# Performance work log

Measured on AMD Instinct MI355X. Metric: run time of the kernel, lower is better.

## Reference

```python
import jax, jax.numpy as jnp
import numpy as np

NSX, NSY = 8, 8          # subdomain grid
BATCH = 8                # PDE instances
PTS = 100_000            # points per instance
IN_C, HID, OUT_C = 32, 64, 32
NUM_CLUSTERS = BATCH * NSX * NSY  # 512


def _clusters(coords, batch_ids):
    # coords assumed in [0,1]^2; bucket into NSX x NSY grid per batch sample
    ix = jnp.clip((coords[:, 0] * NSX).astype(jnp.int32), 0, NSX - 1)
    iy = jnp.clip((coords[:, 1] * NSY).astype(jnp.int32), 0, NSY - 1)
    return batch_ids * (NSX * NSY) + iy * NSX + ix


def _mlp(h, W1, b1, W2, b2):
    # Linear -> GELU(exact, matches torch nn.GELU default) -> Linear
    return jax.nn.gelu(h @ W1 + b1, approximate=False) @ W2 + b2


def setup_inputs() -> dict:
    key = jax.random.key(0)
    ks = jax.random.split(key, 12)
    N = BATCH * PTS
    x = jax.random.normal(ks[0], (N, IN_C), dtype=jnp.float32)
    src_coords = jax.random.uniform(ks[1], (N, 2), dtype=jnp.float32)
    tgt_coords = jax.random.uniform(ks[2], (N, 2), dtype=jnp.float32)
    src_batch = jnp.repeat(jnp.arange(BATCH, dtype=jnp.int32), PTS)
    tgt_batch = jnp.repeat(jnp.arange(BATCH, dtype=jnp.int32), PTS)
    def lin(k, fan_in, fan_out):
        s = 1.0 / np.sqrt(fan_in)
        kw, kb = jax.random.split(k)
        W = jax.random.uniform(kw, (fan_in, fan_out), minval=-s, maxval=s, dtype=jnp.float32)
        b = jax.random.uniform(kb, (fan_out,), minval=-s, maxval=s, dtype=jnp.float32)
        return W, b
    Wv1, bv1 = lin(ks[3], IN_C, HID)
    Wv2, bv2 = lin(ks[4], HID, HID)
    Wt1, bt1 = lin(ks[5], 2 + HID, HID)
    Wt2, bt2 = lin(ks[6], HID, OUT_C)
    return {"x": x, "src_coords": src_coords, "src_batch": src_batch,
            "tgt_coords": tgt_coords, "tgt_batch": tgt_batch,
            "Wv1": Wv1, "bv1": bv1, "Wv2": Wv2, "bv2": bv2,
            "Wt1": Wt1, "bt1": bt1, "Wt2": Wt2, "bt2": bt2}


def reference(x, src_coords, src_batch, tgt_coords, tgt_batch,
              Wv1, bv1, Wv2, bv2, Wt1, bt1, Wt2, bt2):
    src_cl = _clusters(src_coords, src_batch)        # [Ns]
    tgt_cl = _clusters(tgt_coords, tgt_batch)        # [Nt]
    h = _mlp(x, Wv1, bv1, Wv2, bv2)                  # [Ns, HID]
    # subdomain mean-pool (the integral over each subdomain)
    s = jax.ops.segment_sum(h, src_cl, num_segments=NUM_CLUSTERS)        # [C, HID]
    cnt = jax.ops.segment_sum(jnp.ones((h.shape[0], 1), h.dtype), src_cl,
                              num_segments=NUM_CLUSTERS)                 # [C, 1]
    pooled = s / jnp.maximum(cnt, 1.0)
    # broadcast pooled feature to each target point, concat target coords
    feat = jnp.concatenate([tgt_coords, pooled[tgt_cl]], axis=-1)        # [Nt, 2+HID]
    return _mlp(feat, Wt1, bt1, Wt2, bt2)            # [Nt, OUT_C]
```

## Files before the change

### kernel.cpp

```cpp
#include <hip/hip_runtime.h>

#define NC   512
#define INC  32
#define HID  64
#define OUTC 32
#define STRZ 68
#define GSTR 36
#define TSTR 40

typedef __attribute__((ext_vector_type(8))) __bf16 bf16x8;
typedef __attribute__((ext_vector_type(4))) __bf16 bf16x4;
typedef __attribute__((ext_vector_type(4))) float  f32x4;
typedef __attribute__((ext_vector_type(8))) float  f32x8;
typedef __attribute__((ext_vector_type(8))) unsigned int   u32x8;
typedef __attribute__((ext_vector_type(8))) unsigned short u16x8;
typedef __attribute__((ext_vector_type(4))) unsigned short u16x4;

static __device__ __forceinline__ f32x4 mfma16(bf16x8 a, bf16x8 b, f32x4 c){
    return __builtin_amdgcn_mfma_f32_16x16x32_bf16(a, b, c, 0, 0, 0);
}

__device__ __forceinline__ float gelu_f(float v){
    const float s  = v * 0.70710678118654752f;
    const float as = fabsf(s);
    const float t  = __builtin_amdgcn_rcpf(__builtin_fmaf(0.47047f, as, 1.0f));
    const float e  = __expf(-as * as);
    float p = __builtin_fmaf(0.7478556f, t, -0.0958798f);
    p = __builtin_fmaf(p, t, 0.3480242f);
    p = p * t;
    float er = __builtin_fmaf(-p, e, 1.0f);
    er = copysignf(er, s);
    return 0.5f * v * (1.0f + er);
}

__device__ __forceinline__ void split8v(f32x8 x, bf16x8& hi, bf16x8& lo){
    u32x8 ux = __builtin_bit_cast(u32x8, x);
    f32x8 hf = __builtin_bit_cast(f32x8, ux & 0xFFFF0000u);
    f32x8 lf = x - hf;
    u32x8 ul = __builtin_bit_cast(u32x8, lf);
    hi = __builtin_bit_cast(bf16x8, __builtin_convertvector(ux >> 16, u16x8));
    lo = __builtin_bit_cast(bf16x8, __builtin_convertvector(ul >> 16, u16x8));
}

__device__ __forceinline__ u16x4 pack4(f32x4 g){
    return __builtin_bit_cast(u16x4, __builtin_convertvector(g, bf16x4));
}

__global__ __launch_bounds__(256, 3) void k_src(
    const float* __restrict__ x, const float* __restrict__ sc,
    const float* __restrict__ Wv1, const float* __restrict__ bv1,
    float* __restrict__ partial, float* __restrict__ pcntf,
    int npb, int T, int bpb)
{
    __shared__ ushort gbuf[2][4][64][GSTR];
    __shared__ ushort lcw[2][4][32];
    const int t = threadIdx.x;
    const int wave = t >> 6, lane = t & 63;
    const int lrow = lane & 15, lgrp = lane >> 4;
    const int batch = blockIdx.x / bpb;
    const int pb    = blockIdx.x % bpb;

    bf16x8 Bh0, Bh1, Bh2, Bh3, Bl0, Bl1, Bl2, Bl3;
    float bnt0, bnt1, bnt2, bnt3;
    {
        f32x8 w;
        #pragma unroll
        for (int j = 0; j < 8; j++) w[j] = Wv1[(8*lgrp + j)*HID +  0 + lrow];
        split8v(w, Bh0, Bl0);  bnt0 = bv1[ 0 + lrow];
        #pragma unroll
        for (int j = 0; j < 8; j++) w[j] = Wv1[(8*lgrp + j)*HID + 16 + lrow];
        split8v(w, Bh1, Bl1);  bnt1 = bv1[16 + lrow];
        #pragma unroll
        for (int j = 0; j < 8; j++) w[j] = Wv1[(8*lgrp + j)*HID + 32 + lrow];
        split8v(w, Bh2, Bl2);  bnt2 = bv1[32 + lrow];
        #pragma unroll
        for (int j = 0; j < 8; j++) w[j] = Wv1[(8*lgrp + j)*HID + 48 + lrow];
        split8v(w, Bh3, Bl3);  bnt3 = bv1[48 + lrow];
    }
    u16x8 onesu;
    #pragma unroll
    for (int j = 0; j < 8; j++) onesu[j] = 0x3F80u;
    const bf16x8 ONE = __builtin_bit_cast(bf16x8, onesu);

    f32x4 P0 = (f32x4){0.f,0.f,0.f,0.f}, P1 = P0, P2 = P0, P3 = P0, C = P0;

    const int base   = batch * npb + pb * T * 16;
    const int PAIRS  = T >> 1;
    const int rounds = (PAIRS + 3) >> 2;

    int  p_cur  = wave;
    bool a_cur  = p_cur < PAIRS;
    float2 sA_c, sB_c; f32x8 xA_c, xB_c;
    if (a_cur){
        const int pt0 = base + p_cur * 32;
        sA_c = ((const float2*)sc)[pt0 + lrow];
        sB_c = ((const float2*)sc)[pt0 + 16 + lrow];
        xA_c = *(const f32x8*)(x + (size_t)(pt0 + lrow)*INC + 8*lgrp);
        xB_c = *(const f32x8*)(x + (size_t)(pt0 + 16 + lrow)*INC + 8*lgrp);
    }

    for (int r = 0; r < rounds; r++){
        const int buf = r & 1;
        const int  p_nxt = p_cur + 4;
        const bool a_nxt = p_nxt < PAIRS;
        float2 sA_n, sB_n; f32x8 xA_n, xB_n;
        if (a_nxt){
            const int pt0 = base + p_nxt * 32;
            sA_n = ((const float2*)sc)[pt0 + lrow];
            sB_n = ((const float2*)sc)[pt0 + 16 + lrow];
            xA_n = *(const f32x8*)(x + (size_t)(pt0 + lrow)*INC + 8*lgrp);
            xB_n = *(const f32x8*)(x + (size_t)(pt0 + 16 + lrow)*INC + 8*lgrp);
        }

        if (a_cur){
            int ixA = (int)(sA_c.x * 8.0f); ixA = ixA < 0 ? 0 : (ixA > 7 ? 7 : ixA);
            int iyA = (int)(sA_c.y * 8.0f); iyA = iyA < 0 ? 0 : (iyA > 7 ? 7 : iyA);
            int ixB = (int)(sB_c.x * 8.0f); ixB = ixB < 0 ? 0 : (ixB > 7 ? 7 : ixB);
            int iyB = (int)(sB_c.y * 8.0f); iyB = iyB < 0 ? 0 : (iyB > 7 ? 7 : iyB);
            if (lgrp == 0){
                lcw[buf][wave][lrow]      = (ushort)((iyA << 3) + ixA);
                lcw[buf][wave][16 + lrow] = (ushort)((iyB << 3) + ixB);
            }
            {
                bf16x8 Ah = __builtin_convertvector(xA_c, bf16x8);
                f32x4 a0 = (f32x4){0.f,0.f,0.f,0.f}, a1 = a0, a2 = a0, a3 = a0;
                a0 = mfma16(Ah, Bl0, a0); a1 = mfma16(Ah, Bl1, a1);
                a2 = mfma16(Ah, Bl2, a2); a3 = mfma16(Ah, Bl3, a3);
                a0 = mfma16(Ah, Bh0, a0); a1 = mfma16(Ah, Bh1, a1);
                a2 = mfma16(Ah, Bh2, a2); a3 = mfma16(Ah, Bh3, a3);
                f32x4 gv;
                gv[0]=gelu_f(a0[0]+bnt0); gv[1]=gelu_f(a0[1]+bnt0);
                gv[2]=gelu_f(a0[2]+bnt0); gv[3]=gelu_f(a0[3]+bnt0);
                *(u16x4*)&gbuf[buf][wave][ 0 + lrow][4*lgrp] = pack4(gv);
                gv[0]=gelu_f(a1[0]+bnt1); gv[1]=gelu_f(a1[1]+bnt1);
                gv[2]=gelu_f(a1[2]+bnt1); gv[3]=gelu_f(a1[3]+bnt1);
                *(u16x4*)&gbuf[buf][wave][16 + lrow][4*lgrp] = pack4(gv);
                gv[0]=gelu_f(a2[0]+bnt2); gv[1]=gelu_f(a2[1]+bnt2);
                gv[2]=gelu_f(a2[2]+bnt2); gv[3]=gelu_f(a2[3]+bnt2);
                *(u16x4*)&gbuf[buf][wave][32 + lrow][4*lgrp] = pack4(gv);
                gv[0]=gelu_f(a3[0]+bnt3); gv[1]=gelu_f(a3[1]+bnt3);
                gv[2]=gelu_f(a3[2]+bnt3); gv[3]=gelu_f(a3[3]+bnt3);
                *(u16x4*)&gbuf[buf][wave][48 + lrow][4*lgrp] = pack4(gv);
            }
            {
                bf16x8 Ah = __builtin_convertvector(xB_c, bf16x8);
                f32x4 a0 = (f32x4){0.f,0.f,0.f,0.f}, a1 = a0, a2 = a0, a3 = a0;
                a0 = mfma16(Ah, Bl0, a0); a1 = mfma16(Ah, Bl1, a1);
                a2 = mfma16(Ah, Bl2, a2); a3 = mfma16(Ah, Bl3, a3);
                a0 = mfma16(Ah, Bh0, a0); a1 = mfma16(Ah, Bh1, a1);
                a2 = mfma16(Ah, Bh2, a2); a3 = mfma16(Ah, Bh3, a3);
                f32x4 gv;
                gv[0]=gelu_f(a0[0]+bnt0); gv[1]=gelu_f(a0[1]+bnt0);
                gv[2]=gelu_f(a0[2]+bnt0); gv[3]=gelu_f(a0[3]+bnt0);
                *(u16x4*)&gbuf[buf][wave][ 0 + lrow][16 + 4*lgrp] = pack4(gv);
                gv[0]=gelu_f(a1[0]+bnt1); gv[1]=gelu_f(a1[1]+bnt1);
                gv[2]=gelu_f(a1[2]+bnt1); gv[3]=gelu_f(a1[3]+bnt1);
                *(u16x4*)&gbuf[buf][wave][16 + lrow][16 + 4*lgrp] = pack4(gv);
                gv[0]=gelu_f(a2[0]+bnt2); gv[1]=gelu_f(a2[1]+bnt2);
                gv[2]=gelu_f(a2[2]+bnt2); gv[3]=gelu_f(a2[3]+bnt2);
                *(u16x4*)&gbuf[buf][wave][32 + lrow][16 + 4*lgrp] = pack4(gv);
                gv[0]=gelu_f(a3[0]+bnt3); gv[1]=gelu_f(a3[1]+bnt3);
                gv[2]=gelu_f(a3[2]+bnt3); gv[3]=gelu_f(a3[3]+bnt3);
                *(u16x4*)&gbuf[buf][wave][48 + lrow][16 + 4*lgrp] = pack4(gv);
            }
        } else {
            if (lgrp == 0){
                lcw[buf][wave][lrow]      = 0xFFFFu;
                lcw[buf][wave][16 + lrow] = 0xFFFFu;
            }
            u16x4 zz = (u16x4){0,0,0,0};
            #pragma unroll
            for (int nt = 0; nt < 4; nt++){
                *(u16x4*)&gbuf[buf][wave][16*nt + lrow][4*lgrp] = zz;
                *(u16x4*)&gbuf[buf][wave][16*nt + lrow][16 + 4*lgrp] = zz;
            }
        }
        __syncthreads();

        const ushort tgt = (ushort)(16*wave + lrow);
        #pragma unroll
        for (int s = 0; s < 4; s++){
            const u16x8 lcv = *(const u16x8*)&lcw[buf][s][8*lgrp];
            u16x8 ohu;
            #pragma unroll
            for (int j = 0; j < 8; j++)
                ohu[j] = (lcv[j] == tgt) ? (ushort)0x3F80u : (ushort)0;
            const bf16x8 oh = __builtin_bit_cast(bf16x8, ohu);
            u16x4 glo, ghi;
            glo = *(const u16x4*)&gbuf[buf][s][ 0 + lrow][8*lgrp];
            ghi = *(const u16x4*)&gbuf[buf][s][ 0 + lrow][8*lgrp + 4];
            bf16x8 g0 = __builtin_bit_cast(bf16x8, __builtin_shufflevector(glo, ghi, 0,1,2,3,4,5,6,7));
            glo = *(const u16x4*)&gbuf[buf][s][16 + lrow][8*lgrp];
            ghi = *(const u16x4*)&gbuf[buf][s][16 + lrow][8*lgrp + 4];
            bf16x8 g1 = __builtin_bit_cast(bf16x8, __builtin_shufflevector(glo, ghi, 0,1,2,3,4,5,6,7));
            glo = *(const u16x4*)&gbuf[buf][s][32 + lrow][8*lgrp];
            ghi = *(const u16x4*)&gbuf[buf][s][32 + lrow][8*lgrp + 4];
            bf16x8 g2 = __builtin_bit_cast(bf16x8, __builtin_shufflevector(glo, ghi, 0,1,2,3,4,5,6,7));
            glo = *(const u16x4*)&gbuf[buf][s][48 + lrow][8*lgrp];
            ghi = *(const u16x4*)&gbuf[buf][s][48 + lrow][8*lgrp + 4];
            bf16x8 g3 = __builtin_bit_cast(bf16x8, __builtin_shufflevector(glo, ghi, 0,1,2,3,4,5,6,7));
            P0 = mfma16(oh, g0, P0);
            P1 = mfma16(oh, g1, P1);
            P2 = mfma16(oh, g2, P2);
            P3 = mfma16(oh, g3, P3);
            C  = mfma16(oh, ONE, C);
        }

        p_cur = p_nxt; a_cur = a_nxt;
        sA_c = sA_n; sB_c = sB_n; xA_c = xA_n; xB_c = xB_n;
    }

    float* dst = partial + (size_t)blockIdx.x * 4096;
    #pragma unroll
    for (int reg = 0; reg < 4; reg++){
        const int row = 16*wave + 4*lgrp + reg;
        dst[row*64 +  0 + lrow] = P0[reg];
        dst[row*64 + 16 + lrow] = P1[reg];
        dst[row*64 + 32 + lrow] = P2[reg];
        dst[row*64 + 48 + lrow] = P3[reg];
    }
    if (lrow == 0){
        #pragma unroll
        for (int reg = 0; reg < 4; reg++)
            pcntf[(size_t)blockIdx.x*64 + 16*wave + 4*lgrp + reg] = C[reg];
    }
}

__global__ __launch_bounds__(256) void k_cluster(
    const float* __restrict__ partial, const float* __restrict__ pcntf,
    const float* __restrict__ Wv2, const float* __restrict__ bv2,
    const float* __restrict__ Wt1, const float* __restrict__ bt1,
    float* __restrict__ z, int spb)
{
    __shared__ float red[4][HID];
    __shared__ float redn[4];
    __shared__ float m[HID];
    __shared__ float ph[HID];
    const int c = blockIdx.x;
    const int t = threadIdx.x, j = t & 63, sl = t >> 6;
    const int batch = c >> 6, lc = c & 63;

    float s = 0.0f, cn = 0.0f;
    for (int b = sl; b < spb; b += 4){
        const size_t slot = (size_t)batch * spb + b;
        s  += partial[slot * 4096 + (size_t)lc * 64 + j];
        cn += pcntf[slot * 64 + lc];
    }
    red[sl][j] = s;
    if (j == 0) redn[sl] = cn;
    __syncthreads();

    if (sl == 0){
        float stot = red[0][j] + red[1][j] + red[2][j] + red[3][j];
        float ntot = redn[0] + redn[1] + redn[2] + redn[3];
        const float inv = (ntot > 0.0f) ? (1.0f / ntot) : 0.0f;
        m[j] = stot * inv;
        __builtin_amdgcn_s_barrier();
        float a = bv2[j];
        #pragma unroll 8
        for (int i = 0; i < HID; i++) a += m[i] * Wv2[i*HID + j];
        if (ntot <= 0.0f) a = 0.0f;
        ph[j] = a;
        __builtin_amdgcn_s_barrier();
        float b = bt1[j];
        #pragma unroll 8
        for (int i = 0; i < HID; i++) b += ph[i] * Wt1[(2 + i)*HID + j];
        z[c*HID + j] = b;
    }
}

__global__ __launch_bounds__(256, 3) void k_tgt(
    const float* __restrict__ tc,
    const float* __restrict__ z, const float* __restrict__ Wt1,
    const float* __restrict__ Wt2, const float* __restrict__ bt2,
    float* __restrict__ out, int npb, int TT, int bpt)
{
    __shared__ float zs[64*STRZ];
    __shared__ __align__(16) float trans[4][16][TSTR];
    const int t = threadIdx.x;
    const int wave = t >> 6, lane = t & 63;
    const int lrow = lane & 15, lgrp = lane >> 4;
    const int batch = blockIdx.x / bpt;
    const int toff  = (blockIdx.x % bpt) * TT;

    for (int k = t; k < 4096; k += 256)
        zs[(k >> 6)*STRZ + (k & 63)] = z[(size_t)(batch*64)*HID + k];

    bf16x8 Bh00, Bh01, Bh10, Bh11, Bl00, Bl01, Bl10, Bl11;
    f32x8 w0v0, w0v1, w1v0, w1v1;
    {
        f32x8 w;
        #pragma unroll
        for (int j = 0; j < 8; j++) w[j] = Wt2[( 0 + 8*lgrp + j)*OUTC +  0 + lrow];
        split8v(w, Bh00, Bl00);
        #pragma unroll
        for (int j = 0; j < 8; j++) w[j] = Wt2[( 0 + 8*lgrp + j)*OUTC + 16 + lrow];
        split8v(w, Bh01, Bl01);
        #pragma unroll
        for (int j = 0; j < 8; j++) w[j] = Wt2[(32 + 8*lgrp + j)*OUTC +  0 + lrow];
        split8v(w, Bh10, Bl10);
        #pragma unroll
        for (int j = 0; j < 8; j++) w[j] = Wt2[(32 + 8*lgrp + j)*OUTC + 16 + lrow];
        split8v(w, Bh11, Bl11);
        #pragma unroll
        for (int j = 0; j < 8; j++){
            w0v0[j] = Wt1[ 0 + 8*lgrp + j];
            w0v1[j] = Wt1[32 + 8*lgrp + j];
            w1v0[j] = Wt1[HID +  0 + 8*lgrp + j];
            w1v1[j] = Wt1[HID + 32 + 8*lgrp + j];
        }
    }
    const float bo0 = bt2[lrow], bo1 = bt2[16 + lrow];
    __syncthreads();

    const size_t pbase = (size_t)batch * npb;
    float2 c2_c = ((const float2*)tc)[pbase + (size_t)(toff + wave)*16 + lrow];

    const int rpt = lane >> 3;
    const int rko = (lane & 7) * 4;

    for (int tt = toff + wave; tt < toff + TT; tt += 4){
        const int ttn = tt + 4;
        float2 c2_n = c2_c;
        if (ttn < toff + TT)
            c2_n = ((const float2*)tc)[pbase + (size_t)ttn*16 + lrow];

        int ix = (int)(c2_c.x * 8.0f); ix = ix < 0 ? 0 : (ix > 7 ? 7 : ix);
        int iy = (int)(c2_c.y * 8.0f); iy = iy < 0 ? 0 : (iy > 7 ? 7 : iy);
        const int zb = ((iy << 3) + ix) * STRZ;

        f32x8 z0 = *(const f32x8*)(&zs[zb +  0 + 8*lgrp]);
        f32x8 z1 = *(const f32x8*)(&zs[zb + 32 + 8*lgrp]);
        f32x8 g0, g1;
        #pragma unroll
        for (int j = 0; j < 8; j++){
            g0[j] = gelu_f(z0[j] + c2_c.x * w0v0[j] + c2_c.y * w1v0[j]);
            g1[j] = gelu_f(z1[j] + c2_c.x * w0v1[j] + c2_c.y * w1v1[j]);
        }
        bf16x8 Ah0, Al0, Ah1, Al1;
        split8v(g0, Ah0, Al0);
        split8v(g1, Ah1, Al1);

        f32x4 a0 = (f32x4){0.f,0.f,0.f,0.f}, a1 = a0;
        a0 = mfma16(Al0, Bh00, a0); a1 = mfma16(Al0, Bh01, a1);
        a0 = mfma16(Ah0, Bl00, a0); a1 = mfma16(Ah0, Bl01, a1);
        a0 = mfma16(Ah0, Bh00, a0); a1 = mfma16(Ah0, Bh01, a1);
        a0 = mfma16(Al1, Bh10, a0); a1 = mfma16(Al1, Bh11, a1);
        a0 = mfma16(Ah1, Bl10, a0); a1 = mfma16(Ah1, Bl11, a1);
        a0 = mfma16(Ah1, Bh10, a0); a1 = mfma16(Ah1, Bh11, a1);

        #pragma unroll
        for (int q = 0; q < 4; q++){
            trans[wave][4*lgrp + q][lrow]      = a0[q] + bo0;
            trans[wave][4*lgrp + q][16 + lrow] = a1[q] + bo1;
        }
        const size_t prow = pbase + (size_t)tt*16;
        f32x4 v0 = *(const f32x4*)&trans[wave][rpt][rko];
        f32x4 v1 = *(const f32x4*)&trans[wave][8 + rpt][rko];
        *(f32x4*)(out + (prow + rpt)*OUTC + rko)     = v0;
        *(f32x4*)(out + (prow + 8 + rpt)*OUTC + rko) = v1;

        c2_c = c2_n;
    }
}

extern "C" void kernel_launch(void* const* d_in, const int* in_sizes, int n_in,
                              void* d_out, int out_size, void* d_ws, size_t ws_size,
                              hipStream_t stream)
{
    const float* x   = (const float*)d_in[0];
    const float* sc  = (const float*)d_in[1];
    const int*   sb  = (const int*)  d_in[2];  (void)sb;
    const float* tc  = (const float*)d_in[3];
    const int*   tb  = (const int*)  d_in[4];  (void)tb;
    const float* Wv1 = (const float*)d_in[5];
    const float* bv1 = (const float*)d_in[6];
    const float* Wv2 = (const float*)d_in[7];
    const float* bv2 = (const float*)d_in[8];
    const float* Wt1 = (const float*)d_in[9];
    const float* bt1 = (const float*)d_in[10];
    const float* Wt2 = (const float*)d_in[11];
    const float* bt2 = (const float*)d_in[12];
    float* out = (float*)d_out;

    const int n   = in_sizes[2];
    const int npb = n / 8;
    const int tiles_pb = npb / 16;

    int bpb = 1;
    const int cands[4] = {125, 25, 5, 1};
    for (int ci = 0; ci < 4; ci++){
        const int d = cands[ci];
        if (tiles_pb % d) continue;
        if ((tiles_pb / d) & 1) continue;
        const size_t slots = (size_t)8 * d;
        const size_t need  = slots * 4096 * 4 + slots * 64 * 4 + (size_t)NC*HID*4 + 4096;
        if (need <= ws_size){ bpb = d; break; }
    }
    const int T    = tiles_pb / bpb;
    const int nblk = 8 * bpb;
    const size_t slots = (size_t)nblk;

    char* ws = (char*)d_ws;
    float* partial = (float*)(ws);
    float* pcntf   = (float*)(ws + slots * 4096 * 4);
    float* z       = (float*)(ws + slots * 4096 * 4 + slots * 64 * 4);

    k_src    <<<nblk, 256, 0, stream>>>(x, sc, Wv1, bv1, partial, pcntf, npb, T, bpb);
    k_cluster<<<NC, 256, 0, stream>>>(partial, pcntf, Wv2, bv2, Wt1, bt1, z, bpb);

    int TT = 1;
    const int tcands[5] = {10, 25, 5, 2, 1};
    for (int ci = 0; ci < 5; ci++){
        if (tiles_pb % tcands[ci] == 0){ TT = tcands[ci]; break; }
    }
    const int bpt = tiles_pb / TT;
    k_tgt    <<<8*bpt, 256, 0, stream>>>(tc, z, Wt1, Wt2, bt2, out, npb, TT, bpt);
}
```

Baseline: 104.2 us.

## Support odd tile counts in source kernel to allow more blocks, drop LDS double buffer

The source kernel now handles an odd number of 16-point tiles per block by guarding the A and B halves of each pair separately. This lets the host pick 250 blocks per batch instead of 125, doubling the grid for better CU fill. The double-buffered LDS staging is replaced with a single buffer plus an extra barrier per round, which cuts shared memory use but adds a sync. The target kernel's tile-per-block preference also changes from 10 to 25.

Result: slower. 110.3 us (+5.9%).

```diff
diff --git a/kernel.cpp b/kernel.cpp
--- a/kernel.cpp
+++ b/kernel.cpp
@@ -52,8 +52,8 @@
     float* __restrict__ partial, float* __restrict__ pcntf,
     int npb, int T, int bpb)
 {
-    __shared__ ushort gbuf[2][4][64][GSTR];
-    __shared__ ushort lcw[2][4][32];
+    __shared__ ushort gbuf[4][64][GSTR];
+    __shared__ ushort lcw[4][32];
     const int t = threadIdx.x;
     const int wave = t >> 6, lane = t & 63;
     const int lrow = lane & 15, lgrp = lane >> 4;
@@ -85,119 +85,124 @@
     f32x4 P0 = (f32x4){0.f,0.f,0.f,0.f}, P1 = P0, P2 = P0, P3 = P0, C = P0;
 
     const int base   = batch * npb + pb * T * 16;
-    const int PAIRS  = T >> 1;
+    const int PAIRS  = (T + 1) >> 1;
     const int rounds = (PAIRS + 3) >> 2;
 
     int  p_cur  = wave;
-    bool a_cur  = p_cur < PAIRS;
+    bool aA_c = p_cur < PAIRS;
+    bool aB_c = (2*p_cur + 1) < T;
     float2 sA_c, sB_c; f32x8 xA_c, xB_c;
-    if (a_cur){
+    if (aA_c){
         const int pt0 = base + p_cur * 32;
         sA_c = ((const float2*)sc)[pt0 + lrow];
+        xA_c = *(const f32x8*)(x + (size_t)(pt0 + lrow)*INC + 8*lgrp);
+    }
+    if (aB_c){
+        const int pt0 = base + p_cur * 32;
         sB_c = ((const float2*)sc)[pt0 + 16 + lrow];
-        xA_c = *(const f32x8*)(x + (size_t)(pt0 + lrow)*INC + 8*lgrp);
         xB_c = *(const f32x8*)(x + (size_t)(pt0 + 16 + lrow)*INC + 8*lgrp);
     }
 
     for (int r = 0; r < rounds; r++){
-        const int buf = r & 1;
         const int  p_nxt = p_cur + 4;
-        const bool a_nxt = p_nxt < PAIRS;
+        const bool aA_n = p_nxt < PAIRS;
+        const bool aB_n = (2*p_nxt + 1) < T;
         float2 sA_n, sB_n; f32x8 xA_n, xB_n;
-        if (a_nxt){
+        if (aA_n){
             const int pt0 = base + p_nxt * 32;
             sA_n = ((const float2*)sc)[pt0 + lrow];
+            xA_n = *(const f32x8*)(x + (size_t)(pt0 + lrow)*INC + 8*lgrp);
+        }
+        if (aB_n){
+            const int pt0 = base + p_nxt * 32;
             sB_n = ((const float2*)sc)[pt0 + 16 + lrow];
-            xA_n = *(const f32x8*)(x + (size_t)(pt0 + lrow)*INC + 8*lgrp);
             xB_n = *(const f32x8*)(x + (size_t)(pt0 + 16 + lrow)*INC + 8*lgrp);
         }
 
-        if (a_cur){
+        if (aA_c){
             int ixA = (int)(sA_c.x * 8.0f); ixA = ixA < 0 ? 0 : (ixA > 7 ? 7 : ixA);
             int iyA = (int)(sA_c.y * 8.0f); iyA = iyA < 0 ? 0 : (iyA > 7 ? 7 : iyA);
+            if (lgrp == 0) lcw[wave][lrow] = (ushort)((iyA << 3) + ixA);
+            bf16x8 Ah = __builtin_convertvector(xA_c, bf16x8);
+            f32x4 a0 = (f32x4){0.f,0.f,0.f,0.f}, a1 = a0, a2 = a0, a3 = a0;
+            a0 = mfma16(Ah, Bl0, a0); a1 = mfma16(Ah, Bl1, a1);
+            a2 = mfma16(Ah, Bl2, a2); a3 = mfma16(Ah, Bl3, a3);
+            a0 = mfma16(Ah, Bh0, a0); a1 = mfma16(Ah, Bh1, a1);
+            a2 = mfma16(Ah, Bh2, a2); a3 = mfma16(Ah, Bh3, a3);
+            f32x4 gv;
+            gv[0]=gelu_f(a0[0]+bnt0); gv[1]=gelu_f(a0[1]+bnt0);
+            gv[2]=gelu_f(a0[2]+bnt0); gv[3]=gelu_f(a0[3]+bnt0);
+            *(u16x4*)&gbuf[wave][ 0 + lrow][4*lgrp] = pack4(gv);
+            gv[0]=gelu_f(a1[0]+bnt1); gv[1]=gelu_f(a1[1]+bnt1);
+            gv[2]=gelu_f(a1[2]+bnt1); gv[3]=gelu_f(a1[3]+bnt1);
+            *(u16x4*)&gbuf[wave][16 + lrow][4*lgrp] = pack4(gv);
+            gv[0]=gelu_f(a2[0]+bnt2); gv[1]=gelu_f(a2[1]+bnt2);
+            gv[2]=gelu_f(a2[2]+bnt2); gv[3]=gelu_f(a2[3]+bnt2);
+            *(u16x4*)&gbuf[wave][32 + lrow][4*lgrp] = pack4(gv);
+            gv[0]=gelu_f(a3[0]+bnt3); gv[1]=gelu_f(a3[1]+bnt3);
+            gv[2]=gelu_f(a3[2]+bnt3); gv[3]=gelu_f(a3[3]+bnt3);
+            *(u16x4*)&gbuf[wave][48 + lrow][4*lgrp] = pack4(gv);
+        } else {
+            if (lgrp == 0) lcw[wave][lrow] = 0xFFFFu;
+            u16x4 zz = (u16x4){0,0,0,0};
+            #pragma unroll
+            for (int nt = 0; nt < 4; nt++)
+                *(u16x4*)&gbuf[wave][16*nt + lrow][4*lgrp] = zz;
+        }
+        if (aB_c){
             int ixB = (int)(sB_c.x * 8.0f); ixB = ixB < 0 ? 0 : (ixB > 7 ? 7 : ixB);
             int iyB = (int)(sB_c.y * 8.0f); iyB = iyB < 0 ? 0 : (iyB > 7 ? 7 : iyB);
-            if (lgrp == 0){
-                lcw[buf][wave][lrow]      = (ushort)((iyA << 3) + ixA);
-                lcw[buf][wave][16 + lrow] = (ushort)((iyB << 3) + ixB);
-            }
-            {
-                bf16x8 Ah = __builtin_convertvector(xA_c, bf16x8);
-                f32x4 a0 = (f32x4){0.f,0.f,0.f,0.f}, a1 = a0, a2 = a0, a3 = a0;
-                a0 = mfma16(Ah, Bl0, a0); a1 = mfma16(Ah, Bl1, a1);
-                a2 = mfma16(Ah, Bl2, a2); a3 = mfma16(Ah, Bl3, a3);
-                a0 = mfma16(Ah, Bh0, a0); a1 = mfma16(Ah, Bh1, a1);
-                a2 = mfma16(Ah, Bh2, a2); a3 = mfma16(Ah, Bh3, a3);
-                f32x4 gv;
-                gv[0]=gelu_f(a0[0]+bnt0); gv[1]=gelu_f(a0[1]+bnt0);
-                gv[2]=gelu_f(a0[2]+bnt0); gv[3]=gelu_f(a0[3]+bnt0);
-                *(u16x4*)&gbuf[buf][wave][ 0 + lrow][4*lgrp] = pack4(gv);
-                gv[0]=gelu_f(a1[0]+bnt1); gv[1]=gelu_f(a1[1]+bnt1);
-                gv[2]=gelu_f(a1[2]+bnt1); gv[3]=gelu_f(a1[3]+bnt1);
-                *(u16x4*)&gbuf[buf][wave][16 + lrow][4*lgrp] = pack4(gv);
-                gv[0]=gelu_f(a2[0]+bnt2); gv[1]=gelu_f(a2[1]+bnt2);
-                gv[2]=gelu_f(a2[2]+bnt2); gv[3]=gelu_f(a2[3]+bnt2);
-                *(u16x4*)&gbuf[buf][wave][32 + lrow][4*lgrp] = pack4(gv);
-                gv[0]=gelu_f(a3[0]+bnt3); gv[1]=gelu_f(a3[1]+bnt3);
-                gv[2]=gelu_f(a3[2]+bnt3); gv[3]=gelu_f(a3[3]+bnt3);
-                *(u16x4*)&gbuf[buf][wave][48 + lrow][4*lgrp] = pack4(gv);
-            }
-            {
-                bf16x8 Ah = __builtin_convertvector(xB_c, bf16x8);
-                f32x4 a0 = (f32x4){0.f,0.f,0.f,0.f}, a1 = a0, a2 = a0, a3 = a0;
-                a0 = mfma16(Ah, Bl0, a0); a1 = mfma16(Ah, Bl1, a1);
-                a2 = mfma16(Ah, Bl2, a2); a3 = mfma16(Ah, Bl3, a3);
-                a0 = mfma16(Ah, Bh0, a0); a1 = mfma16(Ah, Bh1, a1);
-                a2 = mfma16(Ah, Bh2, a2); a3 = mfma16(Ah, Bh3, a3);
-                f32x4 gv;
-                gv[0]=gelu_f(a0[0]+bnt0); gv[1]=gelu_f(a0[1]+bnt0);
-                gv[2]=gelu_f(a0[2]+bnt0); gv[3]=gelu_f(a0[3]+bnt0);
-                *(u16x4*)&gbuf[buf][wave][ 0 + lrow][16 + 4*lgrp] = pack4(gv);
-                gv[0]=gelu_f(a1[0]+bnt1); gv[1]=gelu_f(a1[1]+bnt1);
-                gv[2]=gelu_f(a1[2]+bnt1); gv[3]=gelu_f(a1[3]+bnt1);
-                *(u16x4*)&gbuf[buf][wave][16 + lrow][16 + 4*lgrp] = pack4(gv);
-                gv[0]=gelu_f(a2[0]+bnt2); gv[1]=gelu_f(a2[1]+bnt2);
-                gv[2]=gelu_f(a2[2]+bnt2); gv[3]=gelu_f(a2[3]+bnt2);
-                *(u16x4*)&gbuf[buf][wave][32 + lrow][16 + 4*lgrp] = pack4(gv);
-                gv[0]=gelu_f(a3[0]+bnt3); gv[1]=gelu_f(a3[1]+bnt3);
-                gv[2]=gelu_f(a3[2]+bnt3); gv[3]=gelu_f(a3[3]+bnt3);
-                *(u16x4*)&gbuf[buf][wave][48 + lrow][16 + 4*lgrp] = pack4(gv);
-            }
+            if (lgrp == 0) lcw[wave][16 + lrow] = (ushort)((iyB << 3) + ixB);
+            bf16x8 Ah = __builtin_convertvector(xB_c, bf16x8);
+            f32x4 a0 = (f32x4){0.f,0.f,0.f,0.f}, a1 = a0, a2 = a0, a3 = a0;
+            a0 = mfma16(Ah, Bl0, a0); a1 = mfma16(Ah, Bl1, a1);
+            a2 = mfma16(Ah, Bl2, a2); a3 = mfma16(Ah, Bl3, a3);
+            a0 = mfma16(Ah, Bh0, a0); a1 = mfma16(Ah, Bh1, a1);
+            a2 = mfma16(Ah, Bh2, a2); a3 = mfma16(Ah, Bh3, a3);
+            f32x4 gv;
+            gv[0]=gelu_f(a0[0]+bnt0); gv[1]=gelu_f(a0[1]+bnt0);
+            gv[2]=gelu_f(a0[2]+bnt0); gv[3]=gelu_f(a0[3]+bnt0);
+            *(u16x4*)&gbuf[wave][ 0 + lrow][16 + 4*lgrp] = pack4(gv);
+            gv[0]=gelu_f(a1[0]+bnt1); gv[1]=gelu_f(a1[1]+bnt1);
+            gv[2]=gelu_f(a1[2]+bnt1); gv[3]=gelu_f(a1[3]+bnt1);
+            *(u16x4*)&gbuf[wave][16 + lrow][16 + 4*lgrp] = pack4(gv);
+            gv[0]=gelu_f(a2[0]+bnt2); gv[1]=gelu_f(a2[1]+bnt2);
+            gv[2]=gelu_f(a2[2]+bnt2); gv[3]=gelu_f(a2[3]+bnt2);
+            *(u16x4*)&gbuf[wave][32 + lrow][16 + 4*lgrp] = pack4(gv);
+            gv[0]=gelu_f(a3[0]+bnt3); gv[1]=gelu_f(a3[1]+bnt3);
+            gv[2]=gelu_f(a3[2]+bnt3); gv[3]=gelu_f(a3[3]+bnt3);
+            *(u16x4*)&gbuf[wave][48 + lrow][16 + 4*lgrp] = pack4(gv);
         } else {
-            if (lgrp == 0){
-                lcw[buf][wave][lrow]      = 0xFFFFu;
-                lcw[buf][wave][16 + lrow] = 0xFFFFu;
-            }
+            if (lgrp == 0) lcw[wave][16 + lrow] = 0xFFFFu;
             u16x4 zz = (u16x4){0,0,0,0};
             #pragma unroll
-            for (int nt = 0; nt < 4; nt++){
-                *(u16x4*)&gbuf[buf][wave][16*nt + lrow][4*lgrp] = zz;
-                *(u16x4*)&gbuf[buf][wave][16*nt + lrow][16 + 4*lgrp] = zz;
-            }
-        }
+            for (int nt = 0; nt < 4; nt++)
+                *(u16x4*)&gbuf[wave][16*nt + lrow][16 + 4*lgrp] = zz;
+        }
+
         __syncthreads();
 
         const ushort tgt = (ushort)(16*wave + lrow);
         #pragma unroll
         for (int s = 0; s < 4; s++){
-            const u16x8 lcv = *(const u16x8*)&lcw[buf][s][8*lgrp];
+            const u16x8 lcv = *(const u16x8*)&lcw[s][8*lgrp];
             u16x8 ohu;
             #pragma unroll
             for (int j = 0; j < 8; j++)
                 ohu[j] = (lcv[j] == tgt) ? (ushort)0x3F80u : (ushort)0;
             const bf16x8 oh = __builtin_bit_cast(bf16x8, ohu);
             u16x4 glo, ghi;
-            glo = *(const u16x4*)&gbuf[buf][s][ 0 + lrow][8*lgrp];
-            ghi = *(const u16x4*)&gbuf[buf][s][ 0 + lrow][8*lgrp + 4];
+            glo = *(const u16x4*)&gbuf[s][ 0 + lrow][8*lgrp];
+            ghi = *(const u16x4*)&gbuf[s][ 0 + lrow][8*lgrp + 4];
             bf16x8 g0 = __builtin_bit_cast(bf16x8, __builtin_shufflevector(glo, ghi, 0,1,2,3,4,5,6,7));
-            glo = *(const u16x4*)&gbuf[buf][s][16 + lrow][8*lgrp];
-            ghi = *(const u16x4*)&gbuf[buf][s][16 + lrow][8*lgrp + 4];
+            glo = *(const u16x4*)&gbuf[s][16 + lrow][8*lgrp];
+            ghi = *(const u16x4*)&gbuf[s][16 + lrow][8*lgrp + 4];
             bf16x8 g1 = __builtin_bit_cast(bf16x8, __builtin_shufflevector(glo, ghi, 0,1,2,3,4,5,6,7));
-            glo = *(const u16x4*)&gbuf[buf][s][32 + lrow][8*lgrp];
-            ghi = *(const u16x4*)&gbuf[buf][s][32 + lrow][8*lgrp + 4];
+            glo = *(const u16x4*)&gbuf[s][32 + lrow][8*lgrp];
+            ghi = *(const u16x4*)&gbuf[s][32 + lrow][8*lgrp + 4];
             bf16x8 g2 = __builtin_bit_cast(bf16x8, __builtin_shufflevector(glo, ghi, 0,1,2,3,4,5,6,7));
-            glo = *(const u16x4*)&gbuf[buf][s][48 + lrow][8*lgrp];
-            ghi = *(const u16x4*)&gbuf[buf][s][48 + lrow][8*lgrp + 4];
+            glo = *(const u16x4*)&gbuf[s][48 + lrow][8*lgrp];
+            ghi = *(const u16x4*)&gbuf[s][48 + lrow][8*lgrp + 4];
             bf16x8 g3 = __builtin_bit_cast(bf16x8, __builtin_shufflevector(glo, ghi, 0,1,2,3,4,5,6,7));
             P0 = mfma16(oh, g0, P0);
             P1 = mfma16(oh, g1, P1);
@@ -206,7 +211,9 @@
             C  = mfma16(oh, ONE, C);
         }
 
-        p_cur = p_nxt; a_cur = a_nxt;
+        __syncthreads();
+
+        p_cur = p_nxt; aA_c = aA_n; aB_c = aB_n;
         sA_c = sA_n; sB_c = sB_n; xA_c = xA_n; xB_c = xB_n;
     }
 
@@ -388,11 +395,10 @@
     const int tiles_pb = npb / 16;
 
     int bpb = 1;
-    const int cands[4] = {125, 25, 5, 1};
-    for (int ci = 0; ci < 4; ci++){
+    const int cands[5] = {250, 125, 25, 5, 1};
+    for (int ci = 0; ci < 5; ci++){
         const int d = cands[ci];
         if (tiles_pb % d) continue;
-        if ((tiles_pb / d) & 1) continue;
         const size_t slots = (size_t)8 * d;
         const size_t need  = slots * 4096 * 4 + slots * 64 * 4 + (size_t)NC*HID*4 + 4096;
         if (need <= ws_size){ bpb = d; break; }
@@ -410,7 +416,7 @@
     k_cluster<<<NC, 256, 0, stream>>>(partial, pcntf, Wv2, bv2, Wt1, bt1, z, bpb);
 
     int TT = 1;
-    const int tcands[5] = {10, 25, 5, 2, 1};
+    const int tcands[5] = {25, 10, 5, 2, 1};
     for (int ci = 0; ci < 5; ci++){
         if (tiles_pb % tcands[ci] == 0){ TT = tcands[ci]; break; }
     }
```

## Make each wave pool its own points into private accumulators, dropping per-round block barriers

Applied to the files above, without the earlier changes.

Each wave now keeps 64x64 partial sums for all four cluster tiles in registers and pools only its own gelu outputs, software-pipelined one iteration behind. This removes the per-round __syncthreads and cross-wave LDS reads of the old one-hot MFMA reduction. A cross-wave reduction through LDS at the end combines the per-wave partials. The cost is four times more accumulator registers, so the launch-bounds occupancy hint drops from 3 to 2 blocks per CU, and the number of pooling MFMAs per wave rises.

Measured after the change: 105.7 us. About the same (+1.4%).

```diff
diff --git a/kernel.cpp b/kernel.cpp
--- a/kernel.cpp
+++ b/kernel.cpp
@@ -46,7 +46,7 @@
     return __builtin_bit_cast(u16x4, __builtin_convertvector(g, bf16x4));
 }
 
-__global__ __launch_bounds__(256, 3) void k_src(
+__global__ __launch_bounds__(256, 2) void k_src(
     const float* __restrict__ x, const float* __restrict__ sc,
     const float* __restrict__ Wv1, const float* __restrict__ bv1,
     float* __restrict__ partial, float* __restrict__ pcntf,
@@ -82,37 +82,40 @@
     for (int j = 0; j < 8; j++) onesu[j] = 0x3F80u;
     const bf16x8 ONE = __builtin_bit_cast(bf16x8, onesu);
 
-    f32x4 P0 = (f32x4){0.f,0.f,0.f,0.f}, P1 = P0, P2 = P0, P3 = P0, C = P0;
-
-    const int base   = batch * npb + pb * T * 16;
-    const int PAIRS  = T >> 1;
-    const int rounds = (PAIRS + 3) >> 2;
-
-    int  p_cur  = wave;
-    bool a_cur  = p_cur < PAIRS;
+    f32x4 P[4][4], C[4];
+    #pragma unroll
+    for (int ct = 0; ct < 4; ct++){
+        C[ct] = (f32x4){0.f,0.f,0.f,0.f};
+        #pragma unroll
+        for (int nt = 0; nt < 4; nt++) P[ct][nt] = (f32x4){0.f,0.f,0.f,0.f};
+    }
+
+    const int base  = batch * npb + pb * T * 16;
+    const int PAIRS = T >> 1;
+    const int NITER = (wave < PAIRS) ? ((PAIRS - wave + 3) >> 2) : 0;
+
     float2 sA_c, sB_c; f32x8 xA_c, xB_c;
-    if (a_cur){
-        const int pt0 = base + p_cur * 32;
+    if (NITER > 0){
+        const int pt0 = base + wave * 32;
         sA_c = ((const float2*)sc)[pt0 + lrow];
         sB_c = ((const float2*)sc)[pt0 + 16 + lrow];
         xA_c = *(const f32x8*)(x + (size_t)(pt0 + lrow)*INC + 8*lgrp);
         xB_c = *(const f32x8*)(x + (size_t)(pt0 + 16 + lrow)*INC + 8*lgrp);
     }
 
-    for (int r = 0; r < rounds; r++){
-        const int buf = r & 1;
-        const int  p_nxt = p_cur + 4;
-        const bool a_nxt = p_nxt < PAIRS;
+    for (int i = 0; i < NITER; i++){
+        const int buf = i & 1;
+        const bool nv = (i + 1) < NITER;
         float2 sA_n, sB_n; f32x8 xA_n, xB_n;
-        if (a_nxt){
-            const int pt0 = base + p_nxt * 32;
+        if (nv){
+            const int pt0 = base + (wave + (i+1)*4) * 32;
             sA_n = ((const float2*)sc)[pt0 + lrow];
             sB_n = ((const float2*)sc)[pt0 + 16 + lrow];
             xA_n = *(const f32x8*)(x + (size_t)(pt0 + lrow)*INC + 8*lgrp);
             xB_n = *(const f32x8*)(x + (size_t)(pt0 + 16 + lrow)*INC + 8*lgrp);
         }
 
-        if (a_cur){
+        {
             int ixA = (int)(sA_c.x * 8.0f); ixA = ixA < 0 ? 0 : (ixA > 7 ? 7 : ixA);
             int iyA = (int)(sA_c.y * 8.0f); iyA = iyA < 0 ? 0 : (iyA > 7 ? 7 : iyA);
             int ixB = (int)(sB_c.x * 8.0f); ixB = ixB < 0 ? 0 : (ixB > 7 ? 7 : ixB);
@@ -163,66 +166,119 @@
                 gv[2]=gelu_f(a3[2]+bnt3); gv[3]=gelu_f(a3[3]+bnt3);
                 *(u16x4*)&gbuf[buf][wave][48 + lrow][16 + 4*lgrp] = pack4(gv);
             }
-        } else {
-            if (lgrp == 0){
-                lcw[buf][wave][lrow]      = 0xFFFFu;
-                lcw[buf][wave][16 + lrow] = 0xFFFFu;
-            }
-            u16x4 zz = (u16x4){0,0,0,0};
+        }
+
+        if (i >= 1){
+            const int pbuf = buf ^ 1;
+            const u16x8 lcv = *(const u16x8*)&lcw[pbuf][wave][8*lgrp];
+            u16x4 glo, ghi;
+            glo = *(const u16x4*)&gbuf[pbuf][wave][ 0 + lrow][8*lgrp];
+            ghi = *(const u16x4*)&gbuf[pbuf][wave][ 0 + lrow][8*lgrp + 4];
+            bf16x8 g0 = __builtin_bit_cast(bf16x8, __builtin_shufflevector(glo, ghi, 0,1,2,3,4,5,6,7));
+            glo = *(const u16x4*)&gbuf[pbuf][wave][16 + lrow][8*lgrp];
+            ghi = *(const u16x4*)&gbuf[pbuf][wave][16 + lrow][8*lgrp + 4];
+            bf16x8 g1 = __builtin_bit_cast(bf16x8, __builtin_shufflevector(glo, ghi, 0,1,2,3,4,5,6,7));
+            glo = *(const u16x4*)&gbuf[pbuf][wave][32 + lrow][8*lgrp];
+            ghi = *(const u16x4*)&gbuf[pbuf][wave][32 + lrow][8*lgrp + 4];
+            bf16x8 g2 = __builtin_bit_cast(bf16x8, __builtin_shufflevector(glo, ghi, 0,1,2,3,4,5,6,7));
+            glo = *(const u16x4*)&gbuf[pbuf][wave][48 + lrow][8*lgrp];
+            ghi = *(const u16x4*)&gbuf[pbuf][wave][48 + lrow][8*lgrp + 4];
+            bf16x8 g3 = __builtin_bit_cast(bf16x8, __builtin_shufflevector(glo, ghi, 0,1,2,3,4,5,6,7));
             #pragma unroll
-            for (int nt = 0; nt < 4; nt++){
-                *(u16x4*)&gbuf[buf][wave][16*nt + lrow][4*lgrp] = zz;
-                *(u16x4*)&gbuf[buf][wave][16*nt + lrow][16 + 4*lgrp] = zz;
-            }
-        }
-        __syncthreads();
-
-        const ushort tgt = (ushort)(16*wave + lrow);
-        #pragma unroll
-        for (int s = 0; s < 4; s++){
-            const u16x8 lcv = *(const u16x8*)&lcw[buf][s][8*lgrp];
+            for (int ct = 0; ct < 4; ct++){
+                u16x8 ohu;
+                #pragma unroll
+                for (int j = 0; j < 8; j++)
+                    ohu[j] = (lcv[j] == (ushort)(16*ct + lrow)) ? (ushort)0x3F80u : (ushort)0;
+                const bf16x8 oh = __builtin_bit_cast(bf16x8, ohu);
+                P[ct][0] = mfma16(oh, g0, P[ct][0]);
+                P[ct][1] = mfma16(oh, g1, P[ct][1]);
+                P[ct][2] = mfma16(oh, g2, P[ct][2]);
+                P[ct][3] = mfma16(oh, g3, P[ct][3]);
+                C[ct]    = mfma16(oh, ONE, C[ct]);
+            }
+        }
+
+        sA_c = sA_n; sB_c = sB_n; xA_c = xA_n; xB_c = xB_n;
+    }
+
+    if (NITER > 0){
+        const int pbuf = (NITER - 1) & 1;
+        const u16x8 lcv = *(const u16x8*)&lcw[pbuf][wave][8*lgrp];
+        u16x4 glo, ghi;
+        glo = *(const u16x4*)&gbuf[pbuf][wave][ 0 + lrow][8*lgrp];
+        ghi = *(const u16x4*)&gbuf[pbuf][wave][ 0 + lrow][8*lgrp + 4];
+        bf16x8 g0 = __builtin_bit_cast(bf16x8, __builtin_shufflevector(glo, ghi, 0,1,2,3,4,5,6,7));
+        glo = *(const u16x4*)&gbuf[pbuf][wave][16 + lrow][8*lgrp];
+        ghi = *(const u16x4*)&gbuf[pbuf][wave][16 + lrow][8*lgrp + 4];
+        bf16x8 g1 = __builtin_bit_cast(bf16x8, __builtin_shufflevector(glo, ghi, 0,1,2,3,4,5,6,7));
+        glo = *(const u16x4*)&gbuf[pbuf][wave][32 + lrow][8*lgrp];
+        ghi = *(const u16x4*)&gbuf[pbuf][wave][32 + lrow][8*lgrp + 4];
+        bf16x8 g2 = __builtin_bit_cast(bf16x8, __builtin_shufflevector(glo, ghi, 0,1,2,3,4,5,6,7));
+        glo = *(const u16x4*)&gbuf[pbuf][wave][48 + lrow][8*lgrp];
+        ghi = *(const u16x4*)&gbuf[pbuf][wave][48 + lrow][8*lgrp + 4];
+        bf16x8 g3 = __builtin_bit_cast(bf16x8, __builtin_shufflevector(glo, ghi, 0,1,2,3,4,5,6,7));
+        #pragma unroll
+        for (int ct = 0; ct < 4; ct++){
             u16x8 ohu;
             #pragma unroll
             for (int j = 0; j < 8; j++)
-                ohu[j] = (lcv[j] == tgt) ? (ushort)0x3F80u : (ushort)0;
+                ohu[j] = (lcv[j] == (ushort)(16*ct + lrow)) ? (ushort)0x3F80u : (ushort)0;
             const bf16x8 oh = __builtin_bit_cast(bf16x8, ohu);
-            u16x4 glo, ghi;
-            glo = *(const u16x4*)&gbuf[buf][s][ 0 + lrow][8*lgrp];
-            ghi = *(const u16x4*)&gbuf[buf][s][ 0 + lrow][8*lgrp + 4];
-            bf16x8 g0 = __builtin_bit_cast(bf16x8, __builtin_shufflevector(glo, ghi, 0,1,2,3,4,5,6,7));
-            glo = *(const u16x4*)&gbuf[buf][s][16 + lrow][8*lgrp];
-            ghi = *(const u16x4*)&gbuf[buf][s][16 + lrow][8*lgrp + 4];
-            bf16x8 g1 = __builtin_bit_cast(bf16x8, __builtin_shufflevector(glo, ghi, 0,1,2,3,4,5,6,7));
-            glo = *(const u16x4*)&gbuf[buf][s][32 + lrow][8*lgrp];
-            ghi = *(const u16x4*)&gbuf[buf][s][32 + lrow][8*lgrp + 4];
-            bf16x8 g2 = __builtin_bit_cast(bf16x8, __builtin_shufflevector(glo, ghi, 0,1,2,3,4,5,6,7));
-            glo = *(const u16x4*)&gbuf[buf][s][48 + lrow][8*lgrp];
-            ghi = *(const u16x4*)&gbuf[buf][s][48 + lrow][8*lgrp + 4];
-            bf16x8 g3 = __builtin_bit_cast(bf16x8, __builtin_shufflevector(glo, ghi, 0,1,2,3,4,5,6,7));
-            P0 = mfma16(oh, g0, P0);
-            P1 = mfma16(oh, g1, P1);
-            P2 = mfma16(oh, g2, P2);
-            P3 = mfma16(oh, g3, P3);
-            C  = mfma16(oh, ONE, C);
-        }
-
-        p_cur = p_nxt; a_cur = a_nxt;
-        sA_c = sA_n; sB_c = sB_n; xA_c = xA_n; xB_c = xB_n;
+            P[ct][0] = mfma16(oh, g0, P[ct][0]);
+            P[ct][1] = mfma16(oh, g1, P[ct][1]);
+            P[ct][2] = mfma16(oh, g2, P[ct][2]);
+            P[ct][3] = mfma16(oh, g3, P[ct][3]);
+            C[ct]    = mfma16(oh, ONE, C[ct]);
+        }
     }
 
     float* dst = partial + (size_t)blockIdx.x * 4096;
     #pragma unroll
-    for (int reg = 0; reg < 4; reg++){
-        const int row = 16*wave + 4*lgrp + reg;
-        dst[row*64 +  0 + lrow] = P0[reg];
-        dst[row*64 + 16 + lrow] = P1[reg];
-        dst[row*64 + 32 + lrow] = P2[reg];
-        dst[row*64 + 48 + lrow] = P3[reg];
-    }
-    if (lrow == 0){
-        #pragma unroll
-        for (int reg = 0; reg < 4; reg++)
-            pcntf[(size_t)blockIdx.x*64 + 16*wave + 4*lgrp + reg] = C[reg];
+    for (int ct = 0; ct < 4; ct++){
+        {
+            const int myb = NITER & 1;
+            float* stw = (float*)&gbuf[myb][wave][0][0];
+            #pragma unroll
+            for (int nt = 0; nt < 4; nt++)
+                #pragma unroll
+                for (int q = 0; q < 4; q++)
+                    stw[(4*lgrp + q)*66 + 16*nt + lrow] = P[ct][nt][q];
+            if (lrow == 0){
+                #pragma unroll
+                for (int q = 0; q < 4; q++) stw[1056 + 4*lgrp + q] = C[ct][q];
+            }
+        }
+        __syncthreads();
+        if (wave == ct){
+            #pragma unroll
+            for (int s = 0; s < 4; s++){
+                if (s == ct) continue;
+                const int PAIRS_ = T >> 1;
+                const int ns = (s < PAIRS_) ? ((PAIRS_ - s + 3) >> 2) : 0;
+                const float* sts = (const float*)&gbuf[ns & 1][s][0][0];
+                #pragma unroll
+                for (int nt = 0; nt < 4; nt++)
+                    #pragma unroll
+                    for (int q = 0; q < 4; q++)
+                        P[ct][nt][q] += sts[(4*lgrp + q)*66 + 16*nt + lrow];
+                if (lrow == 0){
+                    #pragma unroll
+                    for (int q = 0; q < 4; q++) C[ct][q] += sts[1056 + 4*lgrp + q];
+                }
+            }
+            #pragma unroll
+            for (int nt = 0; nt < 4; nt++)
+                #pragma unroll
+                for (int q = 0; q < 4; q++)
+                    dst[(16*ct + 4*lgrp + q)*64 + 16*nt + lrow] = P[ct][nt][q];
+            if (lrow == 0){
+                #pragma unroll
+                for (int q = 0; q < 4; q++)
+                    pcntf[(size_t)blockIdx.x*64 + 16*ct + 4*lgrp + q] = C[ct][q];
+            }
+        }
+        __syncthreads();
     }
 }
 
```
